# Performance work log

Measured on AMD Instinct MI355X. Metric: run time of the kernel, lower is better.

Reference implementation:

```python
import jax, jax.numpy as jnp
import numpy as np


def setup_inputs() -> dict:
    key = jax.random.key(0)
    ks = jax.random.split(key, 6)
    B, T, D, H = 2, 2048, 1024, 16
    dk = D // H
    s = 0.02
    return {
        "x": jax.random.normal(ks[0], (B, T, D), dtype=jnp.float32),
        "Wq": jax.random.normal(ks[1], (H, dk, dk), dtype=jnp.float32) * s,
        "Wk": jax.random.normal(ks[2], (H, dk, dk), dtype=jnp.float32) * s,
        "Wv": jax.random.normal(ks[3], (H, dk, dk), dtype=jnp.float32) * s,
        "Wp": jax.random.normal(ks[4], (D, D), dtype=jnp.float32) * s,
        "bp": jnp.zeros((D,), dtype=jnp.float32),
    }


def reference(x, Wq, Wk, Wv, Wp, bp):
    B, T, D = x.shape
    H, dk, _ = Wq.shape
    # split into heads: [B, H, T, dk]
    xh = x.reshape(B, T, H, dk).transpose(0, 2, 1, 3)
    # per-head torch Linear (y = x @ W^T), all heads at once
    q = jnp.einsum('bhtd,hkd->bhtk', xh, Wq)
    k = jnp.einsum('bhtd,hkd->bhtk', xh, Wk)
    v = jnp.einsum('bhtd,hkd->bhtk', xh, Wv)
    scale = 1.0 / jnp.sqrt(jnp.float32(dk))  # original divides by sqrt(C) with C == d_k
    scores = jnp.einsum('bhqd,bhkd->bhqk', q, k) * scale
    causal = jnp.tril(jnp.ones((T, T), dtype=bool))
    scores = jnp.where(causal[None, None], scores, -jnp.inf)
    attn = jax.nn.softmax(scores, axis=-1)
    out = jnp.einsum('bhqk,bhkd->bhqd', attn, v)  # [B,H,T,dk]
    out = out.transpose(0, 2, 1, 3).reshape(B, T, D)  # concat heads
    return out @ Wp.T + bp
```

## Files before the change

### kernel.cpp

```cpp
#include <hip/hip_runtime.h>
#include <math.h>

#define B_ 2
#define T_ 2048
#define D_ 1024
#define H_ 16
#define DK 64
#define BH_ (B_*H_)

typedef __attribute__((ext_vector_type(8))) short short8;
typedef __attribute__((ext_vector_type(4))) short bf16x4;
typedef __attribute__((ext_vector_type(4))) float fragC;

#if defined(__HIP_DEVICE_COMPILE__)
#define MFMA16(A,B,C) __builtin_amdgcn_mfma_f32_16x16x16bf16_1k((A),(B),(C),0,0,0)
#else
#define MFMA16(A,B,C) (C)
#endif
#define MFMA32(A,B,C) __builtin_amdgcn_mfma_f32_16x16x32_bf16((A),(B),(C),0,0,0)

__device__ __forceinline__ unsigned short f2bf(float x) {
    union { float f; unsigned u; } c; c.f = x;
    unsigned r = c.u + 0x7fff + ((c.u >> 16) & 1);
    return (unsigned short)(r >> 16);
}

__device__ __forceinline__ unsigned pack2bf(float a, float b) {
    return (unsigned)f2bf(a) | ((unsigned)f2bf(b) << 16);
}

__device__ __forceinline__ unsigned permpack(float a, float b) {
    union { float f; unsigned u; } ca, cb; ca.f = a; cb.f = b;
    return __builtin_amdgcn_perm(cb.u, ca.u, 0x07060302);
}

__device__ __forceinline__ short8 packbf8(float4 a, float4 b) {
    union { short8 v; unsigned u[4]; } r;
    r.u[0] = pack2bf(a.x, a.y); r.u[1] = pack2bf(a.z, a.w);
    r.u[2] = pack2bf(b.x, b.y); r.u[3] = pack2bf(b.z, b.w);
    return r.v;
}

__device__ __forceinline__ void gload_lds16(const void* g, void* l) {
    __builtin_amdgcn_global_load_lds(
        (const __attribute__((address_space(1))) unsigned int*)g,
        (__attribute__((address_space(3))) unsigned int*)l, 16, 0, 0);
}

__global__ __launch_bounds__(256) void cvt_kernel(
    const float* __restrict__ Wp,
    const float* __restrict__ Wq, const float* __restrict__ Wk,
    const float* __restrict__ Wv,
    unsigned short* __restrict__ Wb, unsigned short* __restrict__ wqkvb)
{
    const int gid = blockIdx.x * 256 + threadIdx.x;
    const float* src; unsigned short* dst;
    if (gid < 131072) { src = Wp + (size_t)gid * 8; dst = Wb + (size_t)gid * 8; }
    else              { int e = gid - 131072;
                        int mat = e >> 13, rem = e & 8191;
                        int h = rem >> 9, od = rem & 511;
                        const float* ws = (mat == 0) ? Wq : (mat == 1) ? Wk : Wv;
                        src = ws + ((size_t)(h << 9) + od) * 8;
                        dst = wqkvb + ((size_t)h*1536 + mat*512 + od) * 8; }
    float4 a = *(const float4*)src;
    float4 b = *(const float4*)(src + 4);
    *(uint4*)dst = make_uint4(pack2bf(a.x, a.y), pack2bf(a.z, a.w),
                              pack2bf(b.x, b.y), pack2bf(b.z, b.w));
}

__global__ __launch_bounds__(256) void qkv_kernel(
    const float* __restrict__ x,
    const unsigned short* __restrict__ wqkvb,
    unsigned short* __restrict__ q, unsigned short* __restrict__ k,
    unsigned short* __restrict__ vt)
{
    __shared__ unsigned short Wl[3*64*64];

    const int bh = blockIdx.x;
    const int b  = bh >> 4, h = bh & 15;
    const int t0 = blockIdx.y * 128;
    const int tid = threadIdx.x;
    const int wave = tid >> 6, lane = tid & 63;
    const int n = lane & 15, quad = lane >> 4;

    {
        const unsigned short* wsrc = wqkvb + (size_t)h * 12288;
        #pragma unroll
        for (int j = 0; j < 6; ++j) {
            const int off = (wave*6 + j) * 512 + lane*8;
            gload_lds16(wsrc + off, &Wl[off]);
        }
    }

    const int tw = t0 + wave*32;
    short8 xf[2][2];
    #pragma unroll
    for (int rt = 0; rt < 2; ++rt) {
        const float* xr = &x[((size_t)b*T_ + tw + rt*16 + n)*D_ + h*DK];
        float4 a0 = *(const float4*)&xr[quad*8];
        float4 a1 = *(const float4*)&xr[quad*8 + 4];
        xf[rt][0] = packbf8(a0, a1);
        float4 b0 = *(const float4*)&xr[32 + quad*8];
        float4 b1 = *(const float4*)&xr[32 + quad*8 + 4];
        xf[rt][1] = packbf8(b0, b1);
    }
    __syncthreads();

    const float qsc = 0.125f * 1.44269504088896340736f;
    const int tb0 = blockIdx.y*8 + wave*2;
    #pragma unroll
    for (int mat = 0; mat < 3; ++mat) {
        const int wbase = mat * 4096;
        #pragma unroll
        for (int ct = 0; ct < 4; ++ct) {
            short8 wf0 = *(const short8*)&Wl[wbase + (ct*16 + n)*64 + quad*8];
            short8 wf1 = *(const short8*)&Wl[wbase + (ct*16 + n)*64 + 32 + quad*8];
            #pragma unroll
            for (int rt = 0; rt < 2; ++rt) {
                fragC z = {0.f,0.f,0.f,0.f};
                if (mat < 2) {
                    z = MFMA32(wf0, xf[rt][0], z);
                    z = MFMA32(wf1, xf[rt][1], z);
                    if (mat == 0) {
                        z[0] *= qsc; z[1] *= qsc; z[2] *= qsc; z[3] *= qsc;
                    }
                    unsigned short* dstg = (mat == 0) ? q : k;
                    unsigned short* dp = &dstg[((size_t)bh*128 + tb0 + rt)*1024
                                               + (ct*2 + (quad>>1))*128 + n*8 + (quad&1)*4];
                    *(uint2*)dp = make_uint2(pack2bf(z[0], z[1]), pack2bf(z[2], z[3]));
                } else {
                    z = MFMA32(xf[rt][0], wf0, z);
                    z = MFMA32(xf[rt][1], wf1, z);
                    const int key0 = tw + rt*16;
                    const int ktv = key0 >> 6, ctv = (key0 >> 4) & 3;
                    unsigned short* dp = &vt[(size_t)bh*131072 + ktv*4096
                                             + ct*1024 + ctv*256 + quad*64 + n*4];
                    *(uint2*)dp = make_uint2(pack2bf(z[0], z[1]), pack2bf(z[2], z[3]));
                }
            }
        }
    }
}

__global__ __launch_bounds__(256, 4) void attn_kernel(
    const unsigned short* __restrict__ q, const unsigned short* __restrict__ k,
    const unsigned short* __restrict__ vt, unsigned short* __restrict__ aout)
{
    __shared__ unsigned short Ks[2][4096];
    __shared__ unsigned short Vs[2][4096];

    const int id = blockIdx.x;
    int qt, bh;
    if (id < 512) { bh = id >> 4;         qt = 31 - (id & 15); }
    else          { bh = (id - 512) >> 4; qt = (id - 512) & 15; }

    const int b   = bh >> 4, h = bh & 15;
    const int tid = threadIdx.x;
    const int wave = tid >> 6, lane = tid & 63;
    const int n = lane & 15, quad = lane >> 4;
    const int q0 = qt*64 + wave*16;

    const unsigned short* qb = &q[((size_t)bh*128 + qt*4 + wave)*1024 + n*8];
    short8 qf0 = *(const short8*)&qb[quad*128];
    short8 qf1 = *(const short8*)&qb[(4 + quad)*128];

    fragC o[4];
    #pragma unroll
    for (int dt = 0; dt < 4; ++dt) o[dt] = (fragC){0.f,0.f,0.f,0.f};
    fragC l4 = {0.f,0.f,0.f,0.f};

    bf16x4 ones4;
    #pragma unroll
    for (int j = 0; j < 4; ++j) ones4[j] = (short)0x3F80;

    const unsigned short* kg = &k[(size_t)bh*131072];
    const unsigned short* vg = &vt[(size_t)bh*131072];

    const int nt = qt + 1;
    gload_lds16(kg + tid*8,        &Ks[0][tid*8]);
    gload_lds16(kg + 2048 + tid*8, &Ks[0][2048 + tid*8]);
    gload_lds16(vg + tid*8,        &Vs[0][tid*8]);
    gload_lds16(vg + 2048 + tid*8, &Vs[0][2048 + tid*8]);

    for (int kt = 0; kt < nt; ++kt) {
        __syncthreads();
        if (kt + 1 < nt) {
            const int nb = (kt + 1) & 1;
            const unsigned short* kgn = kg + (size_t)(kt+1)*4096;
            const unsigned short* vgn = vg + (size_t)(kt+1)*4096;
            gload_lds16(kgn + tid*8,        &Ks[nb][tid*8]);
            gload_lds16(kgn + 2048 + tid*8, &Ks[nb][2048 + tid*8]);
            gload_lds16(vgn + tid*8,        &Vs[nb][tid*8]);
            gload_lds16(vgn + 2048 + tid*8, &Vs[nb][2048 + tid*8]);
        }
        const unsigned short* Kb = Ks[kt & 1];
        const unsigned short* Vb = Vs[kt & 1];
        const bool diag = (kt == qt);

        bf16x4 pp[4];
        #pragma unroll
        for (int ct = 0; ct < 4; ++ct) {
            short8 kf0 = *(const short8*)&Kb[ct*1024 + quad*128 + n*8];
            short8 kf1 = *(const short8*)&Kb[ct*1024 + 512 + quad*128 + n*8];
            fragC c = {0.f,0.f,0.f,0.f};
            c = MFMA32(kf0, qf0, c);
            c = MFMA32(kf1, qf1, c);
            float p0 = exp2f(c[0]), p1 = exp2f(c[1]);
            float p2 = exp2f(c[2]), p3 = exp2f(c[3]);
            if (diag) {
                const int lim = (wave*16 + n) - (ct*16 + quad*4);
                if (0 > lim) p0 = 0.f;
                if (1 > lim) p1 = 0.f;
                if (2 > lim) p2 = 0.f;
                if (3 > lim) p3 = 0.f;
            }
            union { bf16x4 v; unsigned u[2]; } pk;
            pk.u[0] = permpack(p0, p1);
            pk.u[1] = permpack(p2, p3);
            pp[ct] = pk.v;
        }
        #pragma unroll
        for (int ct = 0; ct < 4; ++ct)
            l4 = MFMA16(ones4, pp[ct], l4);
        #pragma unroll
        for (int dt = 0; dt < 4; ++dt) {
            #pragma unroll
            for (int ct = 0; ct < 4; ++ct) {
                bf16x4 vf = *(const bf16x4*)&Vb[dt*1024 + ct*256 + quad*64 + n*4];
                o[dt] = MFMA16(vf, pp[ct], o[dt]);
            }
        }
    }

    const float inv = 1.0f / l4[0];
    unsigned short* dp = &aout[((size_t)b*T_ + q0 + n)*D_ + h*DK + quad*4];
    #pragma unroll
    for (int dt = 0; dt < 4; ++dt) {
        *(uint2*)(dp + dt*16) =
            make_uint2(pack2bf(o[dt][0]*inv, o[dt][1]*inv),
                       pack2bf(o[dt][2]*inv, o[dt][3]*inv));
    }
}

__global__ __launch_bounds__(256) void proj_kernel(
    const unsigned short* __restrict__ A, const unsigned short* __restrict__ Wb,
    const float* __restrict__ bp, float* __restrict__ out)
{
    __shared__ unsigned short As[128*64];
    __shared__ unsigned short Bs[128*64];

    const int m0 = blockIdx.x * 128, n0 = blockIdx.y * 128;
    const int tid = threadIdx.x;
    const int wave = tid >> 6, lane = tid & 63;
    const int wm = wave & 1, wn = wave >> 1;
    const int n = lane & 15, quad = lane >> 4;

    const int srow = wave*32 + (lane >> 3);
    const int scol = (lane & 7) * 8;
    const unsigned short* ag = &A [(size_t)(m0 + srow)*1024 + scol];
    const unsigned short* bg = &Wb[(size_t)(n0 + srow)*1024 + scol];
    unsigned short* al = &As[(size_t)srow*64 + scol];
    unsigned short* bl = &Bs[(size_t)srow*64 + scol];

    fragC acc[4][4];
    #pragma unroll
    for (int i = 0; i < 4; ++i)
        #pragma unroll
        for (int j = 0; j < 4; ++j) acc[i][j] = (fragC){0.f,0.f,0.f,0.f};

    for (int kt = 0; kt < 16; ++kt) {
        __syncthreads();
        #pragma unroll
        for (int i = 0; i < 4; ++i) {
            gload_lds16(ag + (size_t)i*8*1024 + kt*64, al + i*8*64);
            gload_lds16(bg + (size_t)i*8*1024 + kt*64, bl + i*8*64);
        }
        __syncthreads();

        #pragma unroll
        for (int kk = 0; kk < 2; ++kk) {
            short8 af[4], bf[4];
            #pragma unroll
            for (int i = 0; i < 4; ++i)
                af[i] = *(const short8*)&As[(wm*64 + i*16 + n)*64 + kk*32 + quad*8];
            #pragma unroll
            for (int j = 0; j < 4; ++j)
                bf[j] = *(const short8*)&Bs[(wn*64 + j*16 + n)*64 + kk*32 + quad*8];
            #pragma unroll
            for (int i = 0; i < 4; ++i)
                #pragma unroll
                for (int j = 0; j < 4; ++j)
                    acc[i][j] = MFMA32(af[i], bf[j], acc[i][j]);
        }
    }

    #pragma unroll
    for (int i = 0; i < 4; ++i) {
        #pragma unroll
        for (int r = 0; r < 4; ++r) {
            const int m = m0 + wm*64 + i*16 + quad*4 + r;
            #pragma unroll
            for (int j = 0; j < 4; ++j) {
                const int col = n0 + wn*64 + j*16 + n;
                out[(size_t)m*1024 + col] = acc[i][j][r] + bp[col];
            }
        }
    }
}

extern "C" void kernel_launch(void* const* d_in, const int* in_sizes, int n_in,
                              void* d_out, int out_size, void* d_ws, size_t ws_size,
                              hipStream_t stream)
{
    const float* x  = (const float*)d_in[0];
    const float* Wq = (const float*)d_in[1];
    const float* Wk = (const float*)d_in[2];
    const float* Wv = (const float*)d_in[3];
    const float* Wp = (const float*)d_in[4];
    const float* bp = (const float*)d_in[5];
    float* out = (float*)d_out;

    const size_t per = (size_t)BH_ * T_ * DK;
    unsigned short* qws   = (unsigned short*)d_ws;
    unsigned short* kws   = qws + per;
    unsigned short* vtws  = kws + per;
    unsigned short* aws   = vtws + per;
    unsigned short* wbws  = aws + per;
    unsigned short* wqkvb = wbws + 1024*1024;

    cvt_kernel<<<dim3(608), 256, 0, stream>>>(Wp, Wq, Wk, Wv, wbws, wqkvb);
    qkv_kernel<<<dim3(BH_, T_/128), 256, 0, stream>>>(x, wqkvb, qws, kws, vtws);
    attn_kernel<<<dim3(1024), 256, 0, stream>>>(qws, kws, vtws, aws);
    proj_kernel<<<dim3(32, 8), 256, 0, stream>>>(aws, wbws, bp, out);
}
```

Before: 150.7 us.

## Split attention key tiles across waves with register-resident K/V and LDS reduction

Restructures the attention kernel so each wave handles all 64 queries of the tile but only every fourth key tile. K and V are loaded straight from global memory into registers, with K prefetched one tile ahead, which removes the shared-memory double buffer and the per-iteration block barrier. Partial outputs and row sums are combined once at the end through shared memory. The V-transpose layout written by the QKV kernel changes so each lane can store and load 16-byte chunks, and the block-to-work mapping is reordered to interleave heads. The cost is much higher register pressure (launch bounds drop to 2 blocks) and poor wave balance when the causal tile count is small.

New measurement: 141.6 us. 1.06x faster.

```diff
diff --git a/kernel.cpp b/kernel.cpp
--- a/kernel.cpp
+++ b/kernel.cpp
@@ -115,10 +115,10 @@
         for (int ct = 0; ct < 4; ++ct) {
             short8 wf0 = *(const short8*)&Wl[wbase + (ct*16 + n)*64 + quad*8];
             short8 wf1 = *(const short8*)&Wl[wbase + (ct*16 + n)*64 + 32 + quad*8];
-            #pragma unroll
-            for (int rt = 0; rt < 2; ++rt) {
-                fragC z = {0.f,0.f,0.f,0.f};
-                if (mat < 2) {
+            if (mat < 2) {
+                #pragma unroll
+                for (int rt = 0; rt < 2; ++rt) {
+                    fragC z = {0.f,0.f,0.f,0.f};
                     z = MFMA32(wf0, xf[rt][0], z);
                     z = MFMA32(wf1, xf[rt][1], z);
                     if (mat == 0) {
@@ -128,117 +128,172 @@
                     unsigned short* dp = &dstg[((size_t)bh*128 + tb0 + rt)*1024
                                                + (ct*2 + (quad>>1))*128 + n*8 + (quad&1)*4];
                     *(uint2*)dp = make_uint2(pack2bf(z[0], z[1]), pack2bf(z[2], z[3]));
-                } else {
-                    z = MFMA32(xf[rt][0], wf0, z);
-                    z = MFMA32(xf[rt][1], wf1, z);
-                    const int key0 = tw + rt*16;
-                    const int ktv = key0 >> 6, ctv = (key0 >> 4) & 3;
-                    unsigned short* dp = &vt[(size_t)bh*131072 + ktv*4096
-                                             + ct*1024 + ctv*256 + quad*64 + n*4];
-                    *(uint2*)dp = make_uint2(pack2bf(z[0], z[1]), pack2bf(z[2], z[3]));
-                }
-            }
-        }
-    }
-}
-
-__global__ __launch_bounds__(256, 4) void attn_kernel(
+                }
+            } else {
+                uint4 pv4;
+                {
+                    fragC z = {0.f,0.f,0.f,0.f};
+                    z = MFMA32(xf[0][0], wf0, z);
+                    z = MFMA32(xf[0][1], wf1, z);
+                    pv4.x = pack2bf(z[0], z[1]); pv4.y = pack2bf(z[2], z[3]);
+                }
+                {
+                    fragC z = {0.f,0.f,0.f,0.f};
+                    z = MFMA32(xf[1][0], wf0, z);
+                    z = MFMA32(xf[1][1], wf1, z);
+                    pv4.z = pack2bf(z[0], z[1]); pv4.w = pack2bf(z[2], z[3]);
+                }
+                const int ktv = tw >> 6, pv = (tw >> 5) & 1;
+                unsigned short* dp = &vt[(size_t)bh*131072 + ktv*4096
+                                         + ct*1024 + pv*512 + lane*8];
+                *(uint4*)dp = pv4;
+            }
+        }
+    }
+}
+
+__global__ __launch_bounds__(256, 2) void attn_kernel(
     const unsigned short* __restrict__ q, const unsigned short* __restrict__ k,
     const unsigned short* __restrict__ vt, unsigned short* __restrict__ aout)
 {
-    __shared__ unsigned short Ks[2][4096];
-    __shared__ unsigned short Vs[2][4096];
+    __shared__ fragC Os[4][4][4][64];
+    __shared__ float Ls[4][4][16];
 
     const int id = blockIdx.x;
-    int qt, bh;
-    if (id < 512) { bh = id >> 4;         qt = 31 - (id & 15); }
-    else          { bh = (id - 512) >> 4; qt = (id - 512) & 15; }
+    const int x  = id & 7, p = id >> 3;
+    const int jj = p & 3, s = p >> 2, g = s & 7, r = s >> 3;
+    const int bh = x*4 + jj;
+    const int qt = (r == 0) ? 31 - g : (r == 1) ? g : (r == 2) ? 23 - g : 8 + g;
 
     const int b   = bh >> 4, h = bh & 15;
     const int tid = threadIdx.x;
-    const int wave = tid >> 6, lane = tid & 63;
+    const int w = tid >> 6, lane = tid & 63;
     const int n = lane & 15, quad = lane >> 4;
-    const int q0 = qt*64 + wave*16;
-
-    const unsigned short* qb = &q[((size_t)bh*128 + qt*4 + wave)*1024 + n*8];
-    short8 qf0 = *(const short8*)&qb[quad*128];
-    short8 qf1 = *(const short8*)&qb[(4 + quad)*128];
-
-    fragC o[4];
-    #pragma unroll
-    for (int dt = 0; dt < 4; ++dt) o[dt] = (fragC){0.f,0.f,0.f,0.f};
-    fragC l4 = {0.f,0.f,0.f,0.f};
+
+    short8 qf[4][2];
+    #pragma unroll
+    for (int qc = 0; qc < 4; ++qc) {
+        const unsigned short* qb = &q[((size_t)bh*128 + qt*4 + qc)*1024 + n*8];
+        qf[qc][0] = *(const short8*)&qb[quad*128];
+        qf[qc][1] = *(const short8*)&qb[(4 + quad)*128];
+    }
+
+    fragC o[4][4];
+    #pragma unroll
+    for (int qc = 0; qc < 4; ++qc)
+        #pragma unroll
+        for (int dt = 0; dt < 4; ++dt) o[qc][dt] = (fragC){0.f,0.f,0.f,0.f};
+    fragC l[4];
+    #pragma unroll
+    for (int qc = 0; qc < 4; ++qc) l[qc] = (fragC){0.f,0.f,0.f,0.f};
 
     bf16x4 ones4;
     #pragma unroll
-    for (int j = 0; j < 4; ++j) ones4[j] = (short)0x3F80;
-
-    const unsigned short* kg = &k[(size_t)bh*131072];
-    const unsigned short* vg = &vt[(size_t)bh*131072];
-
+    for (int jo = 0; jo < 4; ++jo) ones4[jo] = (short)0x3F80;
+
+    const unsigned short* kg = &k[(size_t)bh*131072 + lane*8];
+    const unsigned short* vg = &vt[(size_t)bh*131072 + lane*8];
     const int nt = qt + 1;
-    gload_lds16(kg + tid*8,        &Ks[0][tid*8]);
-    gload_lds16(kg + 2048 + tid*8, &Ks[0][2048 + tid*8]);
-    gload_lds16(vg + tid*8,        &Vs[0][tid*8]);
-    gload_lds16(vg + 2048 + tid*8, &Vs[0][2048 + tid*8]);
-
-    for (int kt = 0; kt < nt; ++kt) {
-        __syncthreads();
-        if (kt + 1 < nt) {
-            const int nb = (kt + 1) & 1;
-            const unsigned short* kgn = kg + (size_t)(kt+1)*4096;
-            const unsigned short* vgn = vg + (size_t)(kt+1)*4096;
-            gload_lds16(kgn + tid*8,        &Ks[nb][tid*8]);
-            gload_lds16(kgn + 2048 + tid*8, &Ks[nb][2048 + tid*8]);
-            gload_lds16(vgn + tid*8,        &Vs[nb][tid*8]);
-            gload_lds16(vgn + 2048 + tid*8, &Vs[nb][2048 + tid*8]);
-        }
-        const unsigned short* Kb = Ks[kt & 1];
-        const unsigned short* Vb = Vs[kt & 1];
-        const bool diag = (kt == qt);
-
-        bf16x4 pp[4];
+
+    short8 kf[4][2];
+    short8 vv[4][2];
+
+    int t = w;
+    if (t < nt) {
         #pragma unroll
         for (int ct = 0; ct < 4; ++ct) {
-            short8 kf0 = *(const short8*)&Kb[ct*1024 + quad*128 + n*8];
-            short8 kf1 = *(const short8*)&Kb[ct*1024 + 512 + quad*128 + n*8];
-            fragC c = {0.f,0.f,0.f,0.f};
-            c = MFMA32(kf0, qf0, c);
-            c = MFMA32(kf1, qf1, c);
-            float p0 = exp2f(c[0]), p1 = exp2f(c[1]);
-            float p2 = exp2f(c[2]), p3 = exp2f(c[3]);
-            if (diag) {
-                const int lim = (wave*16 + n) - (ct*16 + quad*4);
-                if (0 > lim) p0 = 0.f;
-                if (1 > lim) p1 = 0.f;
-                if (2 > lim) p2 = 0.f;
-                if (3 > lim) p3 = 0.f;
-            }
-            union { bf16x4 v; unsigned u[2]; } pk;
-            pk.u[0] = permpack(p0, p1);
-            pk.u[1] = permpack(p2, p3);
-            pp[ct] = pk.v;
-        }
-        #pragma unroll
-        for (int ct = 0; ct < 4; ++ct)
-            l4 = MFMA16(ones4, pp[ct], l4);
+            kf[ct][0] = *(const short8*)&kg[t*4096 + ct*1024];
+            kf[ct][1] = *(const short8*)&kg[t*4096 + ct*1024 + 512];
+        }
+    }
+
+    for (; t < nt; t += 4) {
         #pragma unroll
         for (int dt = 0; dt < 4; ++dt) {
-            #pragma unroll
-            for (int ct = 0; ct < 4; ++ct) {
-                bf16x4 vf = *(const bf16x4*)&Vb[dt*1024 + ct*256 + quad*64 + n*4];
-                o[dt] = MFMA16(vf, pp[ct], o[dt]);
-            }
-        }
-    }
-
-    const float inv = 1.0f / l4[0];
+            vv[dt][0] = *(const short8*)&vg[t*4096 + dt*1024];
+            vv[dt][1] = *(const short8*)&vg[t*4096 + dt*1024 + 512];
+        }
+
+        const bool diag = (t == qt);
+        #pragma unroll
+        for (int qp = 0; qp < 2; ++qp) {
+            bf16x4 pp[2][4];
+            #pragma unroll
+            for (int q2 = 0; q2 < 2; ++q2) {
+                const int qc = qp*2 + q2;
+                #pragma unroll
+                for (int ct = 0; ct < 4; ++ct) {
+                    fragC c = (fragC){0.f,0.f,0.f,0.f};
+                    c = MFMA32(kf[ct][0], qf[qc][0], c);
+                    c = MFMA32(kf[ct][1], qf[qc][1], c);
+                    float p0 = exp2f(c[0]), p1 = exp2f(c[1]);
+                    float p2 = exp2f(c[2]), p3 = exp2f(c[3]);
+                    if (diag) {
+                        const int lim = (qc*16 + n) - (ct*16 + quad*4);
+                        if (0 > lim) p0 = 0.f;
+                        if (1 > lim) p1 = 0.f;
+                        if (2 > lim) p2 = 0.f;
+                        if (3 > lim) p3 = 0.f;
+                    }
+                    union { bf16x4 v; unsigned u[2]; } pk;
+                    pk.u[0] = permpack(p0, p1);
+                    pk.u[1] = permpack(p2, p3);
+                    pp[q2][ct] = pk.v;
+                }
+            }
+
+            if (qp == 1 && t + 4 < nt) {
+                #pragma unroll
+                for (int ct = 0; ct < 4; ++ct) {
+                    kf[ct][0] = *(const short8*)&kg[(t+4)*4096 + ct*1024];
+                    kf[ct][1] = *(const short8*)&kg[(t+4)*4096 + ct*1024 + 512];
+                }
+            }
+
+            #pragma unroll
+            for (int q2 = 0; q2 < 2; ++q2) {
+                const int qc = qp*2 + q2;
+                #pragma unroll
+                for (int ct = 0; ct < 4; ++ct)
+                    l[qc] = MFMA16(ones4, pp[q2][ct], l[qc]);
+            }
+
+            #pragma unroll
+            for (int q2 = 0; q2 < 2; ++q2) {
+                const int qc = qp*2 + q2;
+                #pragma unroll
+                for (int dt = 0; dt < 4; ++dt) {
+                    #pragma unroll
+                    for (int ct = 0; ct < 4; ++ct) {
+                        union { short8 s8; bf16x4 hh[2]; } uv;
+                        uv.s8 = vv[dt][ct >> 1];
+                        o[qc][dt] = MFMA16(uv.hh[ct & 1], pp[q2][ct], o[qc][dt]);
+                    }
+                }
+            }
+        }
+    }
+
+    #pragma unroll
+    for (int qc = 0; qc < 4; ++qc) {
+        #pragma unroll
+        for (int dt = 0; dt < 4; ++dt)
+            Os[w][qc][dt][lane] = o[qc][dt];
+        if (quad == 0) Ls[w][qc][n] = l[qc][0];
+    }
+    __syncthreads();
+
+    const float lsum = Ls[0][w][n] + Ls[1][w][n] + Ls[2][w][n] + Ls[3][w][n];
+    const float inv = 1.0f / lsum;
+    const int q0 = qt*64 + w*16;
     unsigned short* dp = &aout[((size_t)b*T_ + q0 + n)*D_ + h*DK + quad*4];
     #pragma unroll
     for (int dt = 0; dt < 4; ++dt) {
+        fragC sum = Os[0][w][dt][lane] + Os[1][w][dt][lane]
+                  + Os[2][w][dt][lane] + Os[3][w][dt][lane];
         *(uint2*)(dp + dt*16) =
-            make_uint2(pack2bf(o[dt][0]*inv, o[dt][1]*inv),
-                       pack2bf(o[dt][2]*inv, o[dt][3]*inv));
+            make_uint2(pack2bf(sum[0]*inv, sum[1]*inv),
+                       pack2bf(sum[2]*inv, sum[3]*inv));
     }
 }
 
```
